# Performance work log

Measured on AMD Instinct MI355X. Metric: run time of the kernel, lower is better.

Reference implementation:

```python
import jax, jax.numpy as jnp
import numpy as np

N_NODES = 100000
N_EDGES = 3200000
N_ELEMS = 10


def setup_inputs() -> dict:
    key = jax.random.key(0)
    k1, k2, k3, k4, k5 = jax.random.split(key, 5)
    # edge distances in (0.1, 5.1) Angstrom, shape [E, 1]
    x = jax.random.uniform(k1, (N_EDGES, 1), dtype=jnp.float32) * 5.0 + 0.1
    # one-hot-ish node element encoding; only argmax matters
    node_attrs = jax.random.normal(k2, (N_NODES, N_ELEMS), dtype=jnp.float32)
    edge_index = jax.random.randint(k3, (2, N_EDGES), 0, N_NODES)
    # atomic numbers of the chemical species present (1..89)
    atomic_numbers = jax.random.randint(k4, (N_ELEMS,), 1, 90)
    # stand-in for ase.data.covalent_radii (119 entries, ~0.3..2.3 A)
    covalent_radii = jax.random.uniform(k5, (119,), dtype=jnp.float32) * 2.0 + 0.3
    return {
        "x": x,
        "node_attrs": node_attrs,
        "edge_index": edge_index,
        "atomic_numbers": atomic_numbers,
        "covalent_radii": covalent_radii,
    }


def _polynomial_envelope(x, r_max, p):
    # PolynomialCutoff.calculate_envelope, p = 6
    r = x / r_max
    env = (1.0
           - (p + 1.0) * (p + 2.0) / 2.0 * jnp.power(r, p)
           + p * (p + 2.0) * jnp.power(r, p + 1)
           - p * (p + 1.0) / 2.0 * jnp.power(r, p + 2))
    return env * (x < r_max)


def reference(x, node_attrs, edge_index, atomic_numbers, covalent_radii):
    c = jnp.array([0.1818, 0.5099, 0.2802, 0.02817], dtype=jnp.float32)
    p = 6.0
    a_exp = jnp.float32(0.3)
    a_prefactor = jnp.float32(0.4543)

    sender, receiver = edge_index[0], edge_index[1]
    # per-node atomic number from one-hot attrs, [N, 1]
    node_Z = atomic_numbers[jnp.argmax(node_attrs, axis=1)][..., None]
    Z_u = node_Z[sender].astype(jnp.int32)  # [E, 1]
    Z_v = node_Z[receiver].astype(jnp.int32)  # [E, 1]
    Zu_f = Z_u.astype(jnp.float32)
    Zv_f = Z_v.astype(jnp.float32)

    a = a_prefactor * 0.529 / (jnp.power(Zu_f, a_exp) + jnp.power(Zv_f, a_exp))
    r_over_a = x / a  # [E, 1]
    phi = (c[0] * jnp.exp(-3.2 * r_over_a)
           + c[1] * jnp.exp(-0.9423 * r_over_a)
           + c[2] * jnp.exp(-0.4028 * r_over_a)
           + c[3] * jnp.exp(-0.2016 * r_over_a))
    v_edges = 14.3996 * Zu_f * Zv_f / x * phi  # [E, 1]

    r_max = covalent_radii[Z_u] + covalent_radii[Z_v]  # [E, 1]
    envelope = _polynomial_envelope(x, r_max, p)
    v_edges = 0.5 * v_edges * envelope  # [E, 1]

    # scatter-sum edge energies into receiver nodes -> [N]
    V_ZBL = jax.ops.segment_sum(v_edges[:, 0], receiver,
                                num_segments=node_attrs.shape[0])
    return V_ZBL
```

## Files before the change

### kernel.cpp

```cpp
#include <hip/hip_runtime.h>
#include <stdint.h>

#define N_NODES 100000
#define N_ELEM_PAD 100096
#define N_EDGES 3200000
#define N_ELEMS 10
#define N_PAIRS (N_ELEMS * N_ELEMS)

#define NB 256
#define NPB 391
#define SCAT_THREADS 1024
#define EPB 12500
#define NBLK 256
#define NGROUPS (EPB / 4)
#define PREP_BLOCKS 391

#define L_REC   0
#define L_ELEM  50000
#define L_TAB   (50000 + 100096)
#define L_CNT   (L_TAB + 1600)
#define L_OFF   (L_CNT + 1024)
#define LDS_BYTES (L_OFF + 1024)

__global__ __launch_bounds__(256) void prep_kernel(
    const float* __restrict__ node_attrs,
    const int* __restrict__ atomic_numbers,
    const float* __restrict__ covalent_radii,
    uint8_t* __restrict__ node_elem,
    float4* __restrict__ pair_tab) {
  int i = blockIdx.x * 256 + threadIdx.x;

  if (blockIdx.x == 0 && threadIdx.x < N_PAIRS) {
    int t = threadIdx.x;
    int eu = t / N_ELEMS, ev = t % N_ELEMS;
    float Zuf = (float)atomic_numbers[eu];
    float Zvf = (float)atomic_numbers[ev];
    float a = 0.4543f * 0.529f / (powf(Zuf, 0.3f) + powf(Zvf, 0.3f));
    float rmax = covalent_radii[(int)Zuf] + covalent_radii[(int)Zvf];
    pair_tab[t] = make_float4(1.0f / a, 0.5f * 14.3996f * Zuf * Zvf,
                              rmax, 1.0f / rmax);
  }

  if (i < N_NODES) {
    const float2* row = (const float2*)(node_attrs + (size_t)i * N_ELEMS);
    float best = -INFINITY;
    int bj = 0;
#pragma unroll
    for (int k = 0; k < 5; ++k) {
      float2 v = row[k];
      if (v.x > best) { best = v.x; bj = 2 * k; }
      if (v.y > best) { best = v.y; bj = 2 * k + 1; }
    }
    node_elem[i] = (uint8_t)bj;
  }
}

__device__ __forceinline__ float edge_val(float xi, int u, int v,
                                          const uint8_t* s_elem,
                                          const float4* s_tab) {
  int eu = s_elem[u];
  int ev = s_elem[v];
  float4 tb = s_tab[eu * N_ELEMS + ev];
  float roa = xi * tb.x;
  float phi = 0.1818f  * __expf(-3.2f    * roa)
            + 0.5099f  * __expf(-0.9423f * roa)
            + 0.2802f  * __expf(-0.4028f * roa)
            + 0.02817f * __expf(-0.2016f * roa);
  float val = tb.y * phi / xi;
  float r  = xi * tb.w;
  float r2 = r * r;
  float r6 = r2 * r2 * r2;
  float env = 1.0f - 28.0f * r6 + 48.0f * r6 * r - 21.0f * r6 * r2;
  return (xi < tb.z) ? val * env : 0.0f;
}

__global__ __launch_bounds__(SCAT_THREADS) void scatter_kernel(
    const float* __restrict__ x,
    const int* __restrict__ edge_index,
    const uint8_t* __restrict__ node_elem,
    const float4* __restrict__ pair_tab,
    unsigned int* __restrict__ dir,
    unsigned int* __restrict__ records) {
  extern __shared__ char smem[];
  unsigned int* s_rec  = (unsigned int*)(smem + L_REC);
  uint8_t*      s_elem = (uint8_t*)(smem + L_ELEM);
  float4*       s_tab  = (float4*)(smem + L_TAB);
  unsigned int* s_cnt  = (unsigned int*)(smem + L_CNT);
  unsigned int* s_off  = (unsigned int*)(smem + L_OFF);

  int tid = threadIdx.x;

  {
    const uint4* src = (const uint4*)node_elem;
    uint4* dst = (uint4*)s_elem;
    for (int j = tid; j < N_ELEM_PAD / 16; j += SCAT_THREADS) dst[j] = src[j];
  }
  if (tid < N_PAIRS) s_tab[tid] = pair_tab[tid];
  if (tid < NB) s_cnt[tid] = 0u;
  __syncthreads();

  float val[16];
  unsigned int pk[16];

#pragma unroll
  for (int k = 0; k < 4; ++k) {
    int gl = k * SCAT_THREADS + tid;
    bool ok = gl < NGROUPS;
    int e = (blockIdx.x * NGROUPS + gl) * 4;
    float4 xv = make_float4(1, 1, 1, 1);
    int4 uu = make_int4(0, 0, 0, 0), vv = make_int4(0, 0, 0, 0);
    if (ok) {
      xv = *(const float4*)(x + e);
      uu = *(const int4*)(edge_index + e);
      vv = *(const int4*)(edge_index + N_EDGES + e);
    }
    int rv[4] = {vv.x, vv.y, vv.z, vv.w};
    int ru[4] = {uu.x, uu.y, uu.z, uu.w};
    float xs[4] = {xv.x, xv.y, xv.z, xv.w};
#pragma unroll
    for (int c = 0; c < 4; ++c) {
      int j = k * 4 + c;
      if (ok) {
        val[j] = edge_val(xs[c], ru[c], rv[c], s_elem, s_tab);
        unsigned int b = (unsigned int)rv[c] / NPB;
        unsigned int lid = (unsigned int)rv[c] - b * NPB;
        unsigned int r = atomicAdd(&s_cnt[b], 1u);
        pk[j] = (b << 23) | (r << 9) | lid;
      } else {
        pk[j] = 0xFFFFFFFFu;
      }
    }
  }
  __syncthreads();

  if (tid < 64) {
    unsigned int c0 = s_cnt[tid * 4 + 0];
    unsigned int c1 = s_cnt[tid * 4 + 1];
    unsigned int c2 = s_cnt[tid * 4 + 2];
    unsigned int c3 = s_cnt[tid * 4 + 3];
    unsigned int local = c0 + c1 + c2 + c3;
    unsigned int inc = local;
#pragma unroll
    for (int d = 1; d < 64; d <<= 1) {
      unsigned int t = __shfl_up((int)inc, d, 64);
      if (tid >= d) inc += t;
    }
    unsigned int excl = inc - local;
    s_off[tid * 4 + 0] = excl;
    s_off[tid * 4 + 1] = excl + c0;
    s_off[tid * 4 + 2] = excl + c0 + c1;
    s_off[tid * 4 + 3] = excl + c0 + c1 + c2;
  }
  __syncthreads();

  if (tid < NB)
    dir[(size_t)blockIdx.x * NB + tid] = (s_off[tid] << 14) | s_cnt[tid];

#pragma unroll
  for (int j = 0; j < 16; ++j) {
    if (pk[j] != 0xFFFFFFFFu) {
      unsigned int b = pk[j] >> 23;
      unsigned int r = (pk[j] >> 9) & 0x3FFFu;
      unsigned int lid = pk[j] & 0x1FFu;
      s_rec[s_off[b] + r] = (__float_as_uint(val[j]) & ~0x1FFu) | lid;
    }
  }
  __syncthreads();

  {
    uint4* dst = (uint4*)(records + (size_t)blockIdx.x * EPB);
    const uint4* src = (const uint4*)s_rec;
    for (int j = tid; j < EPB / 4; j += SCAT_THREADS) dst[j] = src[j];
  }
}

__global__ __launch_bounds__(1024) void reduce_kernel(
    const unsigned int* __restrict__ dir,
    const unsigned int* __restrict__ records,
    float* __restrict__ out) {
  __shared__ float bins[NPB];
  int b = blockIdx.x, tid = threadIdx.x;

  if (tid < NPB) bins[tid] = 0.0f;
  __syncthreads();

  int seg = tid >> 2;
  int sub = tid & 3;
  unsigned int d = dir[(size_t)seg * NB + b];
  unsigned int c = d & 0x3FFFu;
  unsigned int o = d >> 14;
  const unsigned int* sp = records + (size_t)seg * EPB + o;
  for (unsigned int i = sub; i < c; i += 4) {
    unsigned int rec = sp[i];
    atomicAdd(&bins[rec & 0x1FFu], __uint_as_float(rec & ~0x1FFu));
  }
  __syncthreads();

  int nb0 = b * NPB;
  if (tid < NPB && nb0 + tid < N_NODES) out[nb0 + tid] = bins[tid];
}

extern "C" void kernel_launch(void* const* d_in, const int* in_sizes, int n_in,
                              void* d_out, int out_size, void* d_ws, size_t ws_size,
                              hipStream_t stream) {
  const float* x              = (const float*)d_in[0];
  const float* node_attrs     = (const float*)d_in[1];
  const int*   edge_index     = (const int*)d_in[2];
  const int*   atomic_numbers = (const int*)d_in[3];
  const float* covalent_radii = (const float*)d_in[4];
  float* out = (float*)d_out;

  char* wsp = (char*)d_ws;
  unsigned int* records   = (unsigned int*)wsp;
  unsigned int* dir       = (unsigned int*)(wsp + 12800000);
  float4*       pair_tab  = (float4*)(wsp + 13062144);
  uint8_t*      node_elem = (uint8_t*)(wsp + 13063744);

  prep_kernel<<<PREP_BLOCKS, 256, 0, stream>>>(
      node_attrs, atomic_numbers, covalent_radii, node_elem, pair_tab);

  scatter_kernel<<<NBLK, SCAT_THREADS, LDS_BYTES, stream>>>(
      x, edge_index, node_elem, pair_tab, dir, records);

  reduce_kernel<<<NB, 1024, 0, stream>>>(dir, records, out);
}
```

Before: 118.8 us.

## Pack node elements as nibbles and halve per-block edge chunk to double blocks

Node element indices are now packed two per byte, halving the LDS copy of the element table. That frees enough LDS to cut each scatter block's edge chunk in half and double the grid from 256 to 512 blocks, with the bit fields in the directory and records resized to match. The reduce kernel now has two threads per segment instead of four, because there are twice as many segments. This aims for more resident blocks per CU and better latency hiding, at the cost of each block paying the per-block element-table copy (now half the size, but twice as many blocks) and a larger directory.

```diff
diff --git a/kernel.cpp b/kernel.cpp
--- a/kernel.cpp
+++ b/kernel.cpp
@@ -2,7 +2,7 @@
 #include <stdint.h>
 
 #define N_NODES 100000
-#define N_ELEM_PAD 100096
+#define N_ELEM4 50000
 #define N_EDGES 3200000
 #define N_ELEMS 10
 #define N_PAIRS (N_ELEMS * N_ELEMS)
@@ -10,14 +10,15 @@
 #define NB 256
 #define NPB 391
 #define SCAT_THREADS 1024
-#define EPB 12500
-#define NBLK 256
+#define NBLK 512
+#define EPB 6256
 #define NGROUPS (EPB / 4)
-#define PREP_BLOCKS 391
+#define NG4 (N_EDGES / 4)
+#define PREP_BLOCKS 196
 
 #define L_REC   0
-#define L_ELEM  50000
-#define L_TAB   (50000 + 100096)
+#define L_ELEM  25024
+#define L_TAB   (25024 + 50000)
 #define L_CNT   (L_TAB + 1600)
 #define L_OFF   (L_CNT + 1024)
 #define LDS_BYTES (L_OFF + 1024)
@@ -26,7 +27,7 @@
     const float* __restrict__ node_attrs,
     const int* __restrict__ atomic_numbers,
     const float* __restrict__ covalent_radii,
-    uint8_t* __restrict__ node_elem,
+    uint8_t* __restrict__ node_elem4,
     float4* __restrict__ pair_tab) {
   int i = blockIdx.x * 256 + threadIdx.x;
 
@@ -41,25 +42,35 @@
                               rmax, 1.0f / rmax);
   }
 
-  if (i < N_NODES) {
-    const float2* row = (const float2*)(node_attrs + (size_t)i * N_ELEMS);
-    float best = -INFINITY;
-    int bj = 0;
-#pragma unroll
-    for (int k = 0; k < 5; ++k) {
-      float2 v = row[k];
-      if (v.x > best) { best = v.x; bj = 2 * k; }
-      if (v.y > best) { best = v.y; bj = 2 * k + 1; }
-    }
-    node_elem[i] = (uint8_t)bj;
-  }
+  if (i < N_ELEM4) {
+    unsigned int packed = 0;
+#pragma unroll
+    for (int h = 0; h < 2; ++h) {
+      int node = 2 * i + h;
+      const float2* row = (const float2*)(node_attrs + (size_t)node * N_ELEMS);
+      float best = -INFINITY;
+      int bj = 0;
+#pragma unroll
+      for (int k = 0; k < 5; ++k) {
+        float2 v = row[k];
+        if (v.x > best) { best = v.x; bj = 2 * k; }
+        if (v.y > best) { best = v.y; bj = 2 * k + 1; }
+      }
+      packed |= (unsigned int)bj << (h * 4);
+    }
+    node_elem4[i] = (uint8_t)packed;
+  }
+}
+
+__device__ __forceinline__ int elem_of(const uint8_t* s_elem4, int n) {
+  return (s_elem4[n >> 1] >> ((n & 1) * 4)) & 0xF;
 }
 
 __device__ __forceinline__ float edge_val(float xi, int u, int v,
-                                          const uint8_t* s_elem,
+                                          const uint8_t* s_elem4,
                                           const float4* s_tab) {
-  int eu = s_elem[u];
-  int ev = s_elem[v];
+  int eu = elem_of(s_elem4, u);
+  int ev = elem_of(s_elem4, v);
   float4 tb = s_tab[eu * N_ELEMS + ev];
   float roa = xi * tb.x;
   float phi = 0.1818f  * __expf(-3.2f    * roa)
@@ -77,36 +88,37 @@
 __global__ __launch_bounds__(SCAT_THREADS) void scatter_kernel(
     const float* __restrict__ x,
     const int* __restrict__ edge_index,
-    const uint8_t* __restrict__ node_elem,
+    const uint8_t* __restrict__ node_elem4,
     const float4* __restrict__ pair_tab,
     unsigned int* __restrict__ dir,
     unsigned int* __restrict__ records) {
   extern __shared__ char smem[];
-  unsigned int* s_rec  = (unsigned int*)(smem + L_REC);
-  uint8_t*      s_elem = (uint8_t*)(smem + L_ELEM);
-  float4*       s_tab  = (float4*)(smem + L_TAB);
-  unsigned int* s_cnt  = (unsigned int*)(smem + L_CNT);
-  unsigned int* s_off  = (unsigned int*)(smem + L_OFF);
+  unsigned int* s_rec   = (unsigned int*)(smem + L_REC);
+  uint8_t*      s_elem4 = (uint8_t*)(smem + L_ELEM);
+  float4*       s_tab   = (float4*)(smem + L_TAB);
+  unsigned int* s_cnt   = (unsigned int*)(smem + L_CNT);
+  unsigned int* s_off   = (unsigned int*)(smem + L_OFF);
 
   int tid = threadIdx.x;
 
   {
-    const uint4* src = (const uint4*)node_elem;
-    uint4* dst = (uint4*)s_elem;
-    for (int j = tid; j < N_ELEM_PAD / 16; j += SCAT_THREADS) dst[j] = src[j];
+    const uint4* src = (const uint4*)node_elem4;
+    uint4* dst = (uint4*)s_elem4;
+    for (int j = tid; j < N_ELEM4 / 16; j += SCAT_THREADS) dst[j] = src[j];
   }
   if (tid < N_PAIRS) s_tab[tid] = pair_tab[tid];
   if (tid < NB) s_cnt[tid] = 0u;
   __syncthreads();
 
-  float val[16];
-  unsigned int pk[16];
-
-#pragma unroll
-  for (int k = 0; k < 4; ++k) {
+  float val[8];
+  unsigned int pk[8];
+
+#pragma unroll
+  for (int k = 0; k < 2; ++k) {
     int gl = k * SCAT_THREADS + tid;
-    bool ok = gl < NGROUPS;
-    int e = (blockIdx.x * NGROUPS + gl) * 4;
+    int g  = blockIdx.x * NGROUPS + gl;
+    bool ok = (gl < NGROUPS) && (g < NG4);
+    int e = g * 4;
     float4 xv = make_float4(1, 1, 1, 1);
     int4 uu = make_int4(0, 0, 0, 0), vv = make_int4(0, 0, 0, 0);
     if (ok) {
@@ -121,11 +133,11 @@
     for (int c = 0; c < 4; ++c) {
       int j = k * 4 + c;
       if (ok) {
-        val[j] = edge_val(xs[c], ru[c], rv[c], s_elem, s_tab);
+        val[j] = edge_val(xs[c], ru[c], rv[c], s_elem4, s_tab);
         unsigned int b = (unsigned int)rv[c] / NPB;
         unsigned int lid = (unsigned int)rv[c] - b * NPB;
         unsigned int r = atomicAdd(&s_cnt[b], 1u);
-        pk[j] = (b << 23) | (r << 9) | lid;
+        pk[j] = (b << 22) | (r << 9) | lid;
       } else {
         pk[j] = 0xFFFFFFFFu;
       }
@@ -154,13 +166,13 @@
   __syncthreads();
 
   if (tid < NB)
-    dir[(size_t)blockIdx.x * NB + tid] = (s_off[tid] << 14) | s_cnt[tid];
-
-#pragma unroll
-  for (int j = 0; j < 16; ++j) {
+    dir[(size_t)blockIdx.x * NB + tid] = (s_off[tid] << 13) | s_cnt[tid];
+
+#pragma unroll
+  for (int j = 0; j < 8; ++j) {
     if (pk[j] != 0xFFFFFFFFu) {
-      unsigned int b = pk[j] >> 23;
-      unsigned int r = (pk[j] >> 9) & 0x3FFFu;
+      unsigned int b = pk[j] >> 22;
+      unsigned int r = (pk[j] >> 9) & 0x1FFFu;
       unsigned int lid = pk[j] & 0x1FFu;
       s_rec[s_off[b] + r] = (__float_as_uint(val[j]) & ~0x1FFu) | lid;
     }
@@ -184,13 +196,13 @@
   if (tid < NPB) bins[tid] = 0.0f;
   __syncthreads();
 
-  int seg = tid >> 2;
-  int sub = tid & 3;
+  int seg = tid >> 1;
+  int sub = tid & 1;
   unsigned int d = dir[(size_t)seg * NB + b];
-  unsigned int c = d & 0x3FFFu;
-  unsigned int o = d >> 14;
+  unsigned int c = d & 0x1FFFu;
+  unsigned int o = d >> 13;
   const unsigned int* sp = records + (size_t)seg * EPB + o;
-  for (unsigned int i = sub; i < c; i += 4) {
+  for (unsigned int i = sub; i < c; i += 2) {
     unsigned int rec = sp[i];
     atomicAdd(&bins[rec & 0x1FFu], __uint_as_float(rec & ~0x1FFu));
   }
@@ -211,16 +223,16 @@
   float* out = (float*)d_out;
 
   char* wsp = (char*)d_ws;
-  unsigned int* records   = (unsigned int*)wsp;
-  unsigned int* dir       = (unsigned int*)(wsp + 12800000);
-  float4*       pair_tab  = (float4*)(wsp + 13062144);
-  uint8_t*      node_elem = (uint8_t*)(wsp + 13063744);
+  unsigned int* records    = (unsigned int*)wsp;
+  unsigned int* dir        = (unsigned int*)(wsp + 12812288);
+  float4*       pair_tab   = (float4*)(wsp + 13336576);
+  uint8_t*      node_elem4 = (uint8_t*)(wsp + 13338176);
 
   prep_kernel<<<PREP_BLOCKS, 256, 0, stream>>>(
-      node_attrs, atomic_numbers, covalent_radii, node_elem, pair_tab);
+      node_attrs, atomic_numbers, covalent_radii, node_elem4, pair_tab);
 
   scatter_kernel<<<NBLK, SCAT_THREADS, LDS_BYTES, stream>>>(
-      x, edge_index, node_elem, pair_tab, dir, records);
+      x, edge_index, node_elem4, pair_tab, dir, records);
 
   reduce_kernel<<<NB, 1024, 0, stream>>>(dir, records, out);
 }
```

Result: faster. 115.4 us (-2.9%).
